# Optimization experiments

Measured on AMD Instinct MI355X. Metric: run time of the kernel, lower is better.

Reference implementation:

```python
import jax, jax.numpy as jnp
import numpy as np

SIGMA = 0.05
N_IN, N_OUT, N_HID = 128, 128, 1024
BATCH, LENGTH = 128, 256


def setup_inputs() -> dict:
    key = jax.random.key(0)
    ks = jax.random.split(key, 8)
    input_signal = jax.random.normal(ks[0], (BATCH, LENGTH, N_IN), dtype=jnp.float32)
    hidden = jnp.zeros((BATCH, N_HID), dtype=jnp.float32)
    # learned params (torch nn.Linear stores weight as [out, in])
    W_in = jax.random.normal(ks[1], (N_HID, N_IN), dtype=jnp.float32) / np.sqrt(N_IN)
    W_hh = jax.random.normal(ks[2], (N_HID, N_HID), dtype=jnp.float32) / np.sqrt(N_HID)
    b_hh = jax.random.normal(ks[3], (N_HID,), dtype=jnp.float32) * 0.01
    W_out = jax.random.normal(ks[4], (N_OUT, N_HID), dtype=jnp.float32) / np.sqrt(N_HID)
    # frozen alpha vector (positive, used as sqrt(2/alpha))
    alpha_w = jax.random.uniform(ks[5], (N_HID,), dtype=jnp.float32, minval=5.0, maxval=25.0)
    # per-step noise, shared across batch (torch.randn(n_hid) each step)
    noise = jax.random.normal(ks[6], (LENGTH, N_HID), dtype=jnp.float32)
    return {"input_signal": input_signal, "hidden": hidden, "W_in": W_in,
            "W_hh": W_hh, "b_hh": b_hh, "W_out": W_out,
            "alpha_w": alpha_w, "noise": noise}


def reference(input_signal, hidden, W_in, W_hh, b_hh, W_out, alpha_w, noise):
    # input_signal: [B, T, n_in]; hidden: [B, n_hid]
    x_tbd = jnp.transpose(input_signal, (1, 0, 2))  # [T, B, n_in]
    noise_scale = jnp.sqrt(2.0 / alpha_w) * SIGMA    # [n_hid]

    def step(h, xs):
        x_t, n_t = xs
        pre = x_t @ W_in.T + h @ W_hh.T + b_hh + n_t * noise_scale
        h_new = jax.nn.relu(pre)
        y = h_new @ W_out.T
        return h_new, (h_new, y)

    h_final, (hs, ys) = jax.lax.scan(step, hidden, (x_tbd, noise))
    hidden_list = jnp.transpose(hs, (1, 0, 2))  # [B, T, n_hid]
    output_list = jnp.transpose(ys, (1, 0, 2))  # [B, T, n_out]
    return hidden_list, output_list, h_final
```

## Files before the change

kernel.cpp:

```cpp
#include <hip/hip_runtime.h>
#include <hip/hip_fp16.h>
#include <math.h>


typedef _Float16 half8 __attribute__((ext_vector_type(8)));
typedef float    f32x4 __attribute__((ext_vector_type(4)));
typedef unsigned short ushort8 __attribute__((ext_vector_type(8)));
typedef unsigned long long u64;

#define SIGMA_F 0.05f

constexpr int T_  = 256;
constexpr int B_  = 128;
constexpr int NH  = 1024;
constexpr int NIN = 128;
constexpr int GM  = 8;
constexpr int GN  = 16;
constexpr int MB  = 16;

constexpr u64 TMASK = 0x8000800080008000ULL;
constexpr u64 DMASK = 0x7FFF7FFF7FFF7FFFULL;

constexpr size_t OFF_XT  = 0;
constexpr size_t OFF_NB  = (size_t)T_*B_*NIN*2;
constexpr size_t OFF_WO  = OFF_NB + (size_t)T_*NH*4;
constexpr size_t OFF_HB  = OFF_WO + (size_t)NIN*NH*2;

__device__ __forceinline__ unsigned short f16bits(float v) {
    return __half_as_ushort(__float2half(v));
}
__device__ __forceinline__ u64 ald(const u64* p) {
    return __hip_atomic_load(p, __ATOMIC_RELAXED, __HIP_MEMORY_SCOPE_AGENT);
}
__device__ __forceinline__ void ast(unsigned int* p, unsigned int v) {
    __hip_atomic_store(p, v, __ATOMIC_RELAXED, __HIP_MEMORY_SCOPE_AGENT);
}

__global__ void setup_kernel(const float* __restrict__ X,
                             const float* __restrict__ hidden,
                             const float* __restrict__ b_hh,
                             const float* __restrict__ W_out,
                             const float* __restrict__ alpha_w,
                             const float* __restrict__ noise,
                             unsigned short* __restrict__ Xt,
                             float* __restrict__ NB,
                             unsigned short* __restrict__ Wo,
                             unsigned int* __restrict__ Hb0,
                             unsigned int* __restrict__ Hb1)
{
    int idx = blockIdx.x * 256 + threadIdx.x;
    if (idx < B_ * T_ * NIN) {
        int d = idx & 127, rest = idx >> 7;
        int brow = rest & 127, t = rest >> 7;
        Xt[idx] = f16bits(X[((size_t)brow * T_ + t) * NIN + d]);
    }
    if (idx < T_ * NH) {
        int c = idx & (NH - 1);
        NB[idx] = b_hh[c] + noise[idx] * (sqrtf(2.0f / alpha_w[c]) * SIGMA_F);
    }
    if (idx < NIN * NH) Wo[idx] = f16bits(W_out[idx]);
    if (idx < B_ * NH / 2) {
        unsigned int lo = f16bits(hidden[idx * 2]);
        unsigned int hi = f16bits(hidden[idx * 2 + 1]);
        Hb0[idx] = (lo | (hi << 16)) & 0x7FFF7FFFu;
        Hb1[idx] = 0x80008000u;
    }
}

__global__ __launch_bounds__(256, 1) void rnn_step_kernel(
    const float* __restrict__ W_hh, const float* __restrict__ W_in,
    const unsigned short* __restrict__ Xt, const float* __restrict__ NB,
    unsigned int* __restrict__ Hb0, unsigned int* __restrict__ Hb1,
    float* __restrict__ hidden_list, float* __restrict__ h_final)
{
    __shared__ unsigned short wtile[64 * 960];
    __shared__ unsigned short htile[16 * 1024];

    const int tid = threadIdx.x;
    const int m = blockIdx.x / GN;
    const int n = blockIdx.x % GN;

    const int wave = tid >> 6, lane = tid & 63;
    const int l15 = lane & 15, lk = lane >> 4;
    const int rowA = m * MB + l15;
    const int colW = wave * 16 + l15;
    const int gcol = n * 64 + colW;

    for (int g = tid; g < 64 * 120; g += 256) {
        int row = g / 120, G = g - row * 120;
        const float* s = W_hh + (size_t)(n * 64 + row) * NH + G * 8;
        half8 h;
        #pragma unroll
        for (int j = 0; j < 8; ++j) h[j] = (_Float16)s[j];
        *(half8*)&wtile[row * 960 + ((G ^ (row & 7)) << 3)] = h;
    }

    auto cvt8 = [](const float* s) {
        half8 h;
        #pragma unroll
        for (int j = 0; j < 8; ++j) h[j] = (_Float16)s[j];
        return h;
    };
    half8 bh30 = cvt8(W_hh + (size_t)gcol * NH + 960 + lk * 8);
    half8 bh31 = cvt8(W_hh + (size_t)gcol * NH + 992 + lk * 8);
    half8 bx[4];
    #pragma unroll
    for (int kx = 0; kx < 4; ++kx)
        bx[kx] = cvt8(W_in + (size_t)gcol * NIN + kx * 32 + lk * 8);
    __syncthreads();

    const int hrow = tid >> 4;
    const int part = tid & 15;

    auto xpart = [&](int t) -> f32x4 {
        f32x4 a = {0.f, 0.f, 0.f, 0.f};
        const ushort8* xp = (const ushort8*)(Xt + ((size_t)t * B_ + rowA) * NIN) + lk;
        #pragma unroll
        for (int kx = 0; kx < 4; ++kx) {
            half8 av = __builtin_bit_cast(half8, xp[kx * 4]);
            a = __builtin_amdgcn_mfma_f32_16x16x32_f16(av, bx[kx], a, 0, 0, 0);
        }
        return a;
    };

    f32x4 accx = xpart(0);

    for (int t = 0; t < T_; ++t) {
        const u64* hp = (const u64*)((t & 1) ? Hb1 : Hb0)
                        + (size_t)(m * MB + hrow) * 256 + part * 2;
        const u64 expq = ((t >> 1) & 1) ? TMASK : 0ULL;
        u64 q[16];
        for (;;) {
            #pragma unroll
            for (int j = 0; j < 8; ++j) {
                q[2*j]   = ald(hp + j * 32);
                q[2*j+1] = ald(hp + j * 32 + 1);
            }
            u64 red = 0;
            #pragma unroll
            for (int i = 0; i < 16; ++i) red |= q[i] ^ expq;
            if ((red & TMASK) == 0ULL) break;
            __builtin_amdgcn_s_sleep(2);
        }

        __syncthreads();

        #pragma unroll
        for (int j = 0; j < 8; ++j) {
            union { u64 w[2]; half8 h; } u;
            u.w[0] = q[2*j]   & DMASK;
            u.w[1] = q[2*j+1] & DMASK;
            int G = j * 16 + part;
            *(half8*)&htile[hrow * 1024 + ((G ^ (hrow & 7)) << 3)] = u.h;
        }

        __syncthreads();

        f32x4 acc = accx;
        #pragma unroll
        for (int ki = 0; ki < 30; ++ki) {
            int G = 4 * ki + lk;
            half8 av = *(const half8*)&htile[l15 * 1024 + ((G ^ (l15 & 7)) << 3)];
            half8 bv = *(const half8*)&wtile[colW * 960 + ((G ^ (colW & 7)) << 3)];
            acc = __builtin_amdgcn_mfma_f32_16x16x32_f16(av, bv, acc, 0, 0, 0);
        }
        {
            int G = 120 + lk;
            half8 av = *(const half8*)&htile[l15 * 1024 + ((G ^ (l15 & 7)) << 3)];
            acc = __builtin_amdgcn_mfma_f32_16x16x32_f16(av, bh30, acc, 0, 0, 0);
            G = 124 + lk;
            av = *(const half8*)&htile[l15 * 1024 + ((G ^ (l15 & 7)) << 3)];
            acc = __builtin_amdgcn_mfma_f32_16x16x32_f16(av, bh31, acc, 0, 0, 0);
        }

        const float nb = NB[t * NH + gcol];
        float hv[4];
        #pragma unroll
        for (int r = 0; r < 4; ++r) {
            float v = acc[r] + nb;
            hv[r] = v > 0.f ? v : 0.f;
        }

        if (t < T_ - 1) {
            unsigned int* hn = (t & 1) ? Hb0 : Hb1;
            const unsigned int tagb = (((t + 1) >> 1) & 1) ? 0x80008000u : 0u;
            #pragma unroll
            for (int r = 0; r < 4; ++r) {
                float other = __shfl_xor(hv[r], 1);
                if (!(lane & 1)) {
                    unsigned int val = (unsigned int)f16bits(hv[r]) |
                                       ((unsigned int)f16bits(other) << 16) | tagb;
                    int brow = m * MB + lk * 4 + r;
                    ast(&hn[(size_t)brow * 512 + (gcol >> 1)], val);
                }
            }
        }

        #pragma unroll
        for (int r = 0; r < 4; ++r) {
            int brow = m * MB + lk * 4 + r;
            hidden_list[((size_t)brow * T_ + t) * NH + gcol] = hv[r];
        }
        if (t == T_ - 1) {
            #pragma unroll
            for (int r = 0; r < 4; ++r) {
                int brow = m * MB + lk * 4 + r;
                h_final[(size_t)brow * NH + gcol] = hv[r];
            }
        } else {
            accx = xpart(t + 1);
        }
    }
}

__global__ __launch_bounds__(256, 4) void ygemm_kernel(
    const float* __restrict__ HL, const unsigned short* __restrict__ Wo,
    float* __restrict__ Y)
{
    const int tid = threadIdx.x;
    const int wave = tid >> 6, lane = tid & 63;
    const int l15 = lane & 15, lk = lane >> 4;
    const size_t rowbase = (size_t)blockIdx.x * 64;

    f32x4 acc[4][2] = {};

    #pragma unroll 2
    for (int ki = 0; ki < 32; ++ki) {
        const int k0 = ki * 32 + lk * 8;
        half8 bfr[2];
        #pragma unroll
        for (int nt = 0; nt < 2; ++nt) {
            int ncol = (wave * 2 + nt) * 16 + l15;
            ushort8 braw = *(const ushort8*)(Wo + ncol * NH + k0);
            bfr[nt] = __builtin_bit_cast(half8, braw);
        }
        #pragma unroll
        for (int mt = 0; mt < 4; ++mt) {
            size_t row = rowbase + mt * 16 + l15;
            const float4* ap = (const float4*)(HL + row * NH + k0);
            float4 a0 = ap[0];
            float4 a1 = ap[1];
            half8 a = { (_Float16)a0.x, (_Float16)a0.y, (_Float16)a0.z, (_Float16)a0.w,
                        (_Float16)a1.x, (_Float16)a1.y, (_Float16)a1.z, (_Float16)a1.w };
            #pragma unroll
            for (int nt = 0; nt < 2; ++nt)
                acc[mt][nt] = __builtin_amdgcn_mfma_f32_16x16x32_f16(a, bfr[nt], acc[mt][nt], 0, 0, 0);
        }
    }

    #pragma unroll
    for (int mt = 0; mt < 4; ++mt) {
        #pragma unroll
        for (int nt = 0; nt < 2; ++nt) {
            int ncol = (wave * 2 + nt) * 16 + l15;
            #pragma unroll
            for (int r = 0; r < 4; ++r) {
                size_t row = rowbase + mt * 16 + lk * 4 + r;
                Y[row * NIN + ncol] = acc[mt][nt][r];
            }
        }
    }
}

extern "C" void kernel_launch(void* const* d_in, const int* in_sizes, int n_in,
                              void* d_out, int out_size, void* d_ws, size_t ws_size,
                              hipStream_t stream)
{
    const float* X      = (const float*)d_in[0];
    const float* hidden = (const float*)d_in[1];
    const float* W_in   = (const float*)d_in[2];
    const float* W_hh   = (const float*)d_in[3];
    const float* b_hh   = (const float*)d_in[4];
    const float* W_out  = (const float*)d_in[5];
    const float* alpha  = (const float*)d_in[6];
    const float* noise  = (const float*)d_in[7];

    char* ws = (char*)d_ws;
    unsigned short* Xt = (unsigned short*)(ws + OFF_XT);
    float*          NB = (float*)(ws + OFF_NB);
    unsigned short* Wo = (unsigned short*)(ws + OFF_WO);
    unsigned int*  Hb0 = (unsigned int*)(ws + OFF_HB);
    unsigned int*  Hb1 = Hb0 + (size_t)B_ * NH / 2;

    float* hidden_list = (float*)d_out;
    float* output_list = hidden_list + (size_t)B_ * T_ * NH;
    float* h_final     = output_list + (size_t)B_ * T_ * NIN;

    setup_kernel<<<(B_ * T_ * NIN + 255) / 256, 256, 0, stream>>>(
        X, hidden, b_hh, W_out, alpha, noise, Xt, NB, Wo, Hb0, Hb1);

    rnn_step_kernel<<<GM * GN, 256, 0, stream>>>(
        W_hh, W_in, Xt, NB, Hb0, Hb1, hidden_list, h_final);

    ygemm_kernel<<<(B_ * T_) / 64, 256, 0, stream>>>(
        hidden_list, Wo, output_list);
}
```

Baseline: 841.6 us.

## Process two batch groups per block, interleaving phases to hide cross-block sync latency

The recurrent kernel now launches 64 blocks instead of 128. Each block handles two 16-row batch groups and alternates their per-timestep phases. While one group waits for its neighbours' hidden-state flags, the other group's independent work is meant to fill the gap, and fewer blocks also means fewer participants in the spin-wait exchange. The cost is doubled serial work per block and half as many CUs in use.

```diff
diff --git a/kernel.cpp b/kernel.cpp
--- a/kernel.cpp
+++ b/kernel.cpp
@@ -14,9 +14,8 @@
 constexpr int B_  = 128;
 constexpr int NH  = 1024;
 constexpr int NIN = 128;
-constexpr int GM  = 8;
 constexpr int GN  = 16;
-constexpr int MB  = 16;
+constexpr int NPAIR = 4;
 
 constexpr u64 TMASK = 0x8000800080008000ULL;
 constexpr u64 DMASK = 0x7FFF7FFF7FFF7FFFULL;
@@ -77,12 +76,11 @@
     __shared__ unsigned short htile[16 * 1024];
 
     const int tid = threadIdx.x;
-    const int m = blockIdx.x / GN;
-    const int n = blockIdx.x % GN;
+    const int n = blockIdx.x & 15;
+    const int p = blockIdx.x >> 4;
 
     const int wave = tid >> 6, lane = tid & 63;
     const int l15 = lane & 15, lk = lane >> 4;
-    const int rowA = m * MB + l15;
     const int colW = wave * 16 + l15;
     const int gcol = n * 64 + colW;
 
@@ -112,8 +110,9 @@
     const int hrow = tid >> 4;
     const int part = tid & 15;
 
-    auto xpart = [&](int t) -> f32x4 {
+    auto xpart = [&](int grp, int t) -> f32x4 {
         f32x4 a = {0.f, 0.f, 0.f, 0.f};
+        const int rowA = grp * 16 + l15;
         const ushort8* xp = (const ushort8*)(Xt + ((size_t)t * B_ + rowA) * NIN) + lk;
         #pragma unroll
         for (int kx = 0; kx < 4; ++kx) {
@@ -123,11 +122,9 @@
         return a;
     };
 
-    f32x4 accx = xpart(0);
-
-    for (int t = 0; t < T_; ++t) {
+    auto phase = [&](int grp, int t, f32x4& accx) {
         const u64* hp = (const u64*)((t & 1) ? Hb1 : Hb0)
-                        + (size_t)(m * MB + hrow) * 256 + part * 2;
+                        + (size_t)(grp * 16 + hrow) * 256 + part * 2;
         const u64 expq = ((t >> 1) & 1) ? TMASK : 0ULL;
         u64 q[16];
         for (;;) {
@@ -190,7 +187,7 @@
                 if (!(lane & 1)) {
                     unsigned int val = (unsigned int)f16bits(hv[r]) |
                                        ((unsigned int)f16bits(other) << 16) | tagb;
-                    int brow = m * MB + lk * 4 + r;
+                    int brow = grp * 16 + lk * 4 + r;
                     ast(&hn[(size_t)brow * 512 + (gcol >> 1)], val);
                 }
             }
@@ -198,18 +195,26 @@
 
         #pragma unroll
         for (int r = 0; r < 4; ++r) {
-            int brow = m * MB + lk * 4 + r;
+            int brow = grp * 16 + lk * 4 + r;
             hidden_list[((size_t)brow * T_ + t) * NH + gcol] = hv[r];
         }
         if (t == T_ - 1) {
             #pragma unroll
             for (int r = 0; r < 4; ++r) {
-                int brow = m * MB + lk * 4 + r;
+                int brow = grp * 16 + lk * 4 + r;
                 h_final[(size_t)brow * NH + gcol] = hv[r];
             }
         } else {
-            accx = xpart(t + 1);
-        }
+            accx = xpart(grp, t + 1);
+        }
+    };
+
+    f32x4 accxA = xpart(2 * p, 0);
+    f32x4 accxB = xpart(2 * p + 1, 0);
+
+    for (int t = 0; t < T_; ++t) {
+        phase(2 * p,     t, accxA);
+        phase(2 * p + 1, t, accxB);
     }
 }
 
@@ -289,7 +294,7 @@
     setup_kernel<<<(B_ * T_ * NIN + 255) / 256, 256, 0, stream>>>(
         X, hidden, b_hh, W_out, alpha, noise, Xt, NB, Wo, Hb0, Hb1);
 
-    rnn_step_kernel<<<GM * GN, 256, 0, stream>>>(
+    rnn_step_kernel<<<NPAIR * GN, 256, 0, stream>>>(
         W_hh, W_in, Xt, NB, Hb0, Hb1, hidden_list, h_final);
 
     ygemm_kernel<<<(B_ * T_) / 64, 256, 0, stream>>>(
```

Result: slower. 1.617 ms (+92.1%).

## Pipeline hidden-state polling in four K-segments overlapped with MFMA compute

Applied to the files above, without the earlier changes.

The per-step wait for the previous hidden state is split into four column segments. Each segment is staged into shared memory and multiplied while the next segment is being polled, and the first segment of the next step is prefetched before the output stores and the input projection. This is meant to hide cross-block synchronisation latency behind the recurrent GEMM instead of waiting for the whole row first. It adds more barriers per step (four instead of two) and reorders how lanes map to the hidden buffer, which makes the segment tag checks more complex.

```diff
diff --git a/kernel.cpp b/kernel.cpp
--- a/kernel.cpp
+++ b/kernel.cpp
@@ -80,12 +80,6 @@
     const int m = blockIdx.x / GN;
     const int n = blockIdx.x % GN;
 
-    const int wave = tid >> 6, lane = tid & 63;
-    const int l15 = lane & 15, lk = lane >> 4;
-    const int rowA = m * MB + l15;
-    const int colW = wave * 16 + l15;
-    const int gcol = n * 64 + colW;
-
     for (int g = tid; g < 64 * 120; g += 256) {
         int row = g / 120, G = g - row * 120;
         const float* s = W_hh + (size_t)(n * 64 + row) * NH + G * 8;
@@ -94,6 +88,11 @@
         for (int j = 0; j < 8; ++j) h[j] = (_Float16)s[j];
         *(half8*)&wtile[row * 960 + ((G ^ (row & 7)) << 3)] = h;
     }
+
+    const int wave = tid >> 6, lane = tid & 63;
+    const int l15 = lane & 15, lk = lane >> 4;
+    const int colW = wave * 16 + l15;
+    const int gcol = n * 64 + colW;
 
     auto cvt8 = [](const float* s) {
         half8 h;
@@ -114,6 +113,7 @@
 
     auto xpart = [&](int t) -> f32x4 {
         f32x4 a = {0.f, 0.f, 0.f, 0.f};
+        const int rowA = m * MB + l15;
         const ushort8* xp = (const ushort8*)(Xt + ((size_t)t * B_ + rowA) * NIN) + lk;
         #pragma unroll
         for (int kx = 0; kx < 4; ++kx) {
@@ -123,54 +123,80 @@
         return a;
     };
 
+    auto stage_seg = [&](int s, const u64 q[4]) {
+        union { u64 w[2]; half8 h; } u0, u1;
+        u0.w[0] = q[0] & DMASK; u0.w[1] = q[1] & DMASK;
+        u1.w[0] = q[2] & DMASK; u1.w[1] = q[3] & DMASK;
+        int G0 = 32 * s + 2 * part;
+        *(half8*)&htile[hrow * 1024 + ((G0 ^ (hrow & 7)) << 3)] = u0.h;
+        *(half8*)&htile[hrow * 1024 + (((G0 + 1) ^ (hrow & 7)) << 3)] = u1.h;
+    };
+
     f32x4 accx = xpart(0);
 
+    u64 qa[4];
+    {
+        const u64* hp = (const u64*)Hb0 + (size_t)(m * MB + hrow) * 256 + 4 * part;
+        for (;;) {
+            qa[0] = ald(hp); qa[1] = ald(hp + 1);
+            qa[2] = ald(hp + 2); qa[3] = ald(hp + 3);
+            if (!((qa[0] | qa[1] | qa[2] | qa[3]) & TMASK)) break;
+            __builtin_amdgcn_s_sleep(1);
+        }
+    }
+
     for (int t = 0; t < T_; ++t) {
-        const u64* hp = (const u64*)((t & 1) ? Hb1 : Hb0)
-                        + (size_t)(m * MB + hrow) * 256 + part * 2;
+        const u64* hrowp = (const u64*)((t & 1) ? Hb1 : Hb0)
+                           + (size_t)(m * MB + hrow) * 256 + 4 * part;
         const u64 expq = ((t >> 1) & 1) ? TMASK : 0ULL;
-        u64 q[16];
-        for (;;) {
-            #pragma unroll
-            for (int j = 0; j < 8; ++j) {
-                q[2*j]   = ald(hp + j * 32);
-                q[2*j+1] = ald(hp + j * 32 + 1);
-            }
-            u64 red = 0;
-            #pragma unroll
-            for (int i = 0; i < 16; ++i) red |= q[i] ^ expq;
-            if ((red & TMASK) == 0ULL) break;
-            __builtin_amdgcn_s_sleep(2);
-        }
-
-        __syncthreads();
-
-        #pragma unroll
-        for (int j = 0; j < 8; ++j) {
-            union { u64 w[2]; half8 h; } u;
-            u.w[0] = q[2*j]   & DMASK;
-            u.w[1] = q[2*j+1] & DMASK;
-            int G = j * 16 + part;
-            *(half8*)&htile[hrow * 1024 + ((G ^ (hrow & 7)) << 3)] = u.h;
-        }
-
-        __syncthreads();
-
         f32x4 acc = accx;
-        #pragma unroll
-        for (int ki = 0; ki < 30; ++ki) {
-            int G = 4 * ki + lk;
-            half8 av = *(const half8*)&htile[l15 * 1024 + ((G ^ (l15 & 7)) << 3)];
-            half8 bv = *(const half8*)&wtile[colW * 960 + ((G ^ (colW & 7)) << 3)];
-            acc = __builtin_amdgcn_mfma_f32_16x16x32_f16(av, bv, acc, 0, 0, 0);
-        }
-        {
-            int G = 120 + lk;
-            half8 av = *(const half8*)&htile[l15 * 1024 + ((G ^ (l15 & 7)) << 3)];
-            acc = __builtin_amdgcn_mfma_f32_16x16x32_f16(av, bh30, acc, 0, 0, 0);
-            G = 124 + lk;
-            av = *(const half8*)&htile[l15 * 1024 + ((G ^ (l15 & 7)) << 3)];
-            acc = __builtin_amdgcn_mfma_f32_16x16x32_f16(av, bh31, acc, 0, 0, 0);
+        u64 qb[4];
+
+        #pragma unroll
+        for (int s = 0; s < 4; ++s) {
+            stage_seg(s, qa);
+            if (s < 3) {
+                const u64* p = hrowp + 64 * (s + 1);
+                qb[0] = ald(p);     qb[1] = ald(p + 1);
+                qb[2] = ald(p + 2); qb[3] = ald(p + 3);
+            }
+            __syncthreads();
+
+            if (s < 3) {
+                #pragma unroll
+                for (int j = 0; j < 8; ++j) {
+                    int ki = 8 * s + j;
+                    int G = 4 * ki + lk;
+                    half8 av = *(const half8*)&htile[l15 * 1024 + ((G ^ (l15 & 7)) << 3)];
+                    half8 bv = *(const half8*)&wtile[colW * 960 + ((G ^ (colW & 7)) << 3)];
+                    acc = __builtin_amdgcn_mfma_f32_16x16x32_f16(av, bv, acc, 0, 0, 0);
+                }
+                const u64* p = hrowp + 64 * (s + 1);
+                for (;;) {
+                    u64 red = (qb[0] ^ expq) | (qb[1] ^ expq) |
+                              (qb[2] ^ expq) | (qb[3] ^ expq);
+                    if (!(red & TMASK)) break;
+                    __builtin_amdgcn_s_sleep(1);
+                    qb[0] = ald(p);     qb[1] = ald(p + 1);
+                    qb[2] = ald(p + 2); qb[3] = ald(p + 3);
+                }
+                qa[0] = qb[0]; qa[1] = qb[1]; qa[2] = qb[2]; qa[3] = qb[3];
+            } else {
+                #pragma unroll
+                for (int j = 0; j < 6; ++j) {
+                    int ki = 24 + j;
+                    int G = 4 * ki + lk;
+                    half8 av = *(const half8*)&htile[l15 * 1024 + ((G ^ (l15 & 7)) << 3)];
+                    half8 bv = *(const half8*)&wtile[colW * 960 + ((G ^ (colW & 7)) << 3)];
+                    acc = __builtin_amdgcn_mfma_f32_16x16x32_f16(av, bv, acc, 0, 0, 0);
+                }
+                int G = 120 + lk;
+                half8 av = *(const half8*)&htile[l15 * 1024 + ((G ^ (l15 & 7)) << 3)];
+                acc = __builtin_amdgcn_mfma_f32_16x16x32_f16(av, bh30, acc, 0, 0, 0);
+                G = 124 + lk;
+                av = *(const half8*)&htile[l15 * 1024 + ((G ^ (l15 & 7)) << 3)];
+                acc = __builtin_amdgcn_mfma_f32_16x16x32_f16(av, bh31, acc, 0, 0, 0);
+            }
         }
 
         const float nb = NB[t * NH + gcol];
@@ -194,21 +220,34 @@
                     ast(&hn[(size_t)brow * 512 + (gcol >> 1)], val);
                 }
             }
-        }
-
-        #pragma unroll
-        for (int r = 0; r < 4; ++r) {
-            int brow = m * MB + lk * 4 + r;
-            hidden_list[((size_t)brow * T_ + t) * NH + gcol] = hv[r];
-        }
-        if (t == T_ - 1) {
+            const u64* hp2 = (const u64*)(((t + 1) & 1) ? Hb1 : Hb0)
+                             + (size_t)(m * MB + hrow) * 256 + 4 * part;
+            qa[0] = ald(hp2);     qa[1] = ald(hp2 + 1);
+            qa[2] = ald(hp2 + 2); qa[3] = ald(hp2 + 3);
+
             #pragma unroll
             for (int r = 0; r < 4; ++r) {
                 int brow = m * MB + lk * 4 + r;
+                hidden_list[((size_t)brow * T_ + t) * NH + gcol] = hv[r];
+            }
+            accx = xpart(t + 1);
+
+            const u64 e2 = (((t + 1) >> 1) & 1) ? TMASK : 0ULL;
+            for (;;) {
+                u64 red = (qa[0] ^ e2) | (qa[1] ^ e2) |
+                          (qa[2] ^ e2) | (qa[3] ^ e2);
+                if (!(red & TMASK)) break;
+                __builtin_amdgcn_s_sleep(1);
+                qa[0] = ald(hp2);     qa[1] = ald(hp2 + 1);
+                qa[2] = ald(hp2 + 2); qa[3] = ald(hp2 + 3);
+            }
+        } else {
+            #pragma unroll
+            for (int r = 0; r < 4; ++r) {
+                int brow = m * MB + lk * 4 + r;
+                hidden_list[((size_t)brow * T_ + t) * NH + gcol] = hv[r];
                 h_final[(size_t)brow * NH + gcol] = hv[r];
             }
-        } else {
-            accx = xpart(t + 1);
         }
     }
 }
```

Measured after the change: 1.241 ms. +47.4%, slower.
